# Kernel optimization log

Measured on AMD Instinct MI355X. Metric: run time of the kernel, lower is better.

## Reference

```python
import jax, jax.numpy as jnp
import numpy as np

EPS_COS = 1e-12
EPS_BN = 1e-5


def setup_inputs() -> dict:
    key = jax.random.key(0)
    k1, k2, k3 = jax.random.split(key, 3)
    B, C, H, W = 16384, 3, 32, 32
    K, NUM_CLASSES = 300, 10
    return {
        "x": jax.random.normal(k1, (B, C, H, W), dtype=jnp.float32),
        "w5": jax.random.normal(k2, (K, C, H, W), dtype=jnp.float32),
        "gamma": jnp.ones((K,), dtype=jnp.float32),
        "beta": jnp.zeros((K,), dtype=jnp.float32),
        "w6": jax.random.normal(k3, (NUM_CLASSES, K), dtype=jnp.float32),
    }


def _clp_cos_sim(x, w5):
    # kernel covers the full spatial extent -> one patch per sample.
    B = x.shape[0]
    K = w5.shape[0]
    xf = x.reshape(B, -1)                       # (B, C*H*W)
    wf = w5.reshape(K, -1)                      # (K, C*H*W)
    xn = xf / (jnp.linalg.norm(xf, axis=1, keepdims=True) + EPS_COS)
    wn = wf / (jnp.linalg.norm(wf, axis=1, keepdims=True) + EPS_COS)
    cos = jnp.einsum("bd,kd->bk", xn, wn)      # cosine similarity to each prototype
    return jax.nn.relu(cos)                     # clp: clamp negatives to 0


def reference(x, w5, gamma, beta, w6):
    # fc5: clamped cosine-similarity match against 300 prototypes -> (B, 300, 1, 1)
    fc5 = _clp_cos_sim(x, w5)[:, :, None, None]
    # bn5: BatchNorm2d(300), batch statistics (training-mode forward math)
    mean = jnp.mean(fc5, axis=(0, 2, 3), keepdims=True)
    var = jnp.var(fc5, axis=(0, 2, 3), keepdims=True)
    bn5 = gamma[None, :, None, None] * (fc5 - mean) / jnp.sqrt(var + EPS_BN) \
          + beta[None, :, None, None]
    # fc6: non-competitive 1x1 map 300 -> 10 (dot-product readout), flattened
    fc6 = jnp.einsum("bk,ok->bo", bn5[:, :, 0, 0], w6)   # (B, 10)
    return fc5, bn5, fc6
```

## Files before the change

### kernel.cpp

```cpp
#include <hip/hip_runtime.h>
#include <stdint.h>

#define BATCH 16384
#define DDIM  3072
#define NK    300
#define NKP   320
#define NCLS  10

#define BM 64
#define BN 320
#define BK 64
#define KT (DDIM / BK)

typedef __bf16 bf16x8 __attribute__((ext_vector_type(8)));
typedef float  f32x16 __attribute__((ext_vector_type(16)));

typedef __attribute__((address_space(1))) const void gvoid_as1;
typedef __attribute__((address_space(3))) void lvoid_as3;

__device__ __forceinline__ unsigned f2bf(float f) {
  unsigned u = __float_as_uint(f);
  u += 0x7FFFu + ((u >> 16) & 1u);
  return u >> 16;
}
__device__ __forceinline__ uint4 pack8bf(float4 a, float4 b) {
  uint4 p;
  p.x = f2bf(a.x) | (f2bf(a.y) << 16);
  p.y = f2bf(a.z) | (f2bf(a.w) << 16);
  p.z = f2bf(b.x) | (f2bf(b.y) << 16);
  p.w = f2bf(b.z) | (f2bf(b.w) << 16);
  return p;
}

__global__ __launch_bounds__(256) void prep_w_kernel(
    const float* __restrict__ w5, unsigned short* __restrict__ wn,
    float* __restrict__ rw, float* __restrict__ gsum, float* __restrict__ gsq) {
  const int r = blockIdx.x;
  const int t = threadIdx.x;
  if (r == 0) {
    for (int i = t; i < NKP; i += 256) { gsum[i] = 0.f; gsq[i] = 0.f; }
  }
  unsigned long long* dst = (unsigned long long*)(wn + (size_t)r * DDIM);
  if (r < NK) {
    const float4* src = (const float4*)(w5 + (size_t)r * DDIM);
    float ss = 0.f;
#pragma unroll
    for (int i = 0; i < 3; ++i) {
      float4 v = src[t + i * 256];
      ss += v.x * v.x + v.y * v.y + v.z * v.z + v.w * v.w;
      unsigned lo = f2bf(v.x) | (f2bf(v.y) << 16);
      unsigned hi = f2bf(v.z) | (f2bf(v.w) << 16);
      dst[t + i * 256] = (unsigned long long)lo | ((unsigned long long)hi << 32);
    }
#pragma unroll
    for (int m = 1; m <= 32; m <<= 1) ss += __shfl_xor(ss, m, 64);
    __shared__ float red[4];
    if ((t & 63) == 0) red[t >> 6] = ss;
    __syncthreads();
    if (t == 0) {
      float tot = red[0] + red[1] + red[2] + red[3];
      rw[r] = 1.f / (sqrtf(tot) + 1e-12f);
    }
  } else {
#pragma unroll
    for (int i = 0; i < 3; ++i) dst[t + i * 256] = 0ull;
    if (t == 0) rw[r] = 0.f;
  }
}

__global__ __launch_bounds__(320, 2) void gemm_kernel(
    const float* __restrict__ x, const unsigned short* __restrict__ wn,
    const float* __restrict__ rw, float* __restrict__ fc5,
    float* __restrict__ gsum, float* __restrict__ gsq) {
  __shared__ alignas(16) unsigned short xs[BM * BK];
  __shared__ alignas(16) unsigned short wt[BN * BK];
  __shared__ float rxs[BM];

  const int tid  = threadIdx.x;
  const int lane = tid & 63;
  const int w    = tid >> 6;
  const int m0   = (int)blockIdx.x * BM;

  const int srow = tid >> 2;
  const int sseg = tid & 3;
  const float* xsrc = x + (size_t)(m0 + srow) * DDIM + sseg * 16;
  const int wb0 = srow * 128 + ((((sseg << 1) | 0) ^ (srow & 7)) << 4);
  const int wb1 = srow * 128 + ((((sseg << 1) | 1) ^ (srow & 7)) << 4);

  const int wrow_l = lane >> 3;
  const int wchk_l = (lane & 7) ^ wrow_l;
  const unsigned short* wsrc_base = wn + (size_t)wrow_l * DDIM + wchk_l * 8;

  const int r31   = lane & 31;
  const int khalf = lane >> 5;
  const int rb0 = w * 64 + r31;
  const int rb1 = rb0 + 32;
  const char* aA0 = (const char*)xs + (size_t)r31 * 128;
  const char* aA1 = (const char*)xs + (size_t)(r31 + 32) * 128;
  const char* aB0 = (const char*)wt + (size_t)rb0 * 128;
  const char* aB1 = (const char*)wt + (size_t)rb1 * 128;
  const int swzA = r31 & 7;
  const int swzB0 = rb0 & 7, swzB1 = rb1 & 7;

  f32x16 acc00 = {}, acc01 = {}, acc10 = {}, acc11 = {};
  float ss = 0.f;

  float4 v0, v1, v2, v3;
  if (tid < 256) {
    const float4* p = (const float4*)xsrc;
    v0 = p[0]; v1 = p[1]; v2 = p[2]; v3 = p[3];
  }

  for (int kt = 0; kt < KT; ++kt) {
    if (tid < 256) {
      ss += v0.x*v0.x + v0.y*v0.y + v0.z*v0.z + v0.w*v0.w
          + v1.x*v1.x + v1.y*v1.y + v1.z*v1.z + v1.w*v1.w
          + v2.x*v2.x + v2.y*v2.y + v2.z*v2.z + v2.w*v2.w
          + v3.x*v3.x + v3.y*v3.y + v3.z*v3.z + v3.w*v3.w;
      *(uint4*)((char*)xs + wb0) = pack8bf(v0, v1);
      *(uint4*)((char*)xs + wb1) = pack8bf(v2, v3);
    }
#pragma unroll
    for (int j = 0; j < 8; ++j) {
      const int i = w * 8 + j;
      const unsigned short* src = wsrc_base + (size_t)(8 * i) * DDIM + kt * BK;
      __builtin_amdgcn_global_load_lds((gvoid_as1*)src,
                                       (lvoid_as3*)((char*)wt + i * 1024), 16, 0, 0);
    }
    __syncthreads();
    if (kt + 1 < KT && tid < 256) {
      const float4* p = (const float4*)(xsrc + (size_t)(kt + 1) * BK);
      v0 = p[0]; v1 = p[1]; v2 = p[2]; v3 = p[3];
    }
#pragma unroll
    for (int ks = 0; ks < 4; ++ks) {
      const int c16 = ks * 2 + khalf;
      bf16x8 a0 = *(const bf16x8*)(aA0 + ((c16 ^ swzA) << 4));
      bf16x8 a1 = *(const bf16x8*)(aA1 + ((c16 ^ swzA) << 4));
      bf16x8 b0 = *(const bf16x8*)(aB0 + ((c16 ^ swzB0) << 4));
      bf16x8 b1 = *(const bf16x8*)(aB1 + ((c16 ^ swzB1) << 4));
      acc00 = __builtin_amdgcn_mfma_f32_32x32x16_bf16(a0, b0, acc00, 0, 0, 0);
      acc01 = __builtin_amdgcn_mfma_f32_32x32x16_bf16(a0, b1, acc01, 0, 0, 0);
      acc10 = __builtin_amdgcn_mfma_f32_32x32x16_bf16(a1, b0, acc10, 0, 0, 0);
      acc11 = __builtin_amdgcn_mfma_f32_32x32x16_bf16(a1, b1, acc11, 0, 0, 0);
    }
    if (kt + 1 < KT) __syncthreads();
  }

  ss += __shfl_xor(ss, 1, 64);
  ss += __shfl_xor(ss, 2, 64);
  if (tid < 256 && sseg == 0) rxs[srow] = 1.f / (sqrtf(ss) + 1e-12f);
  __syncthreads();

  const int kh4 = khalf * 4;
  const int ng0 = w * 64 + r31;
  const int ng1 = ng0 + 32;
  const float rwv0 = rw[ng0];
  const float rwv1 = rw[ng1];
  float s0 = 0.f, q0 = 0.f, s1 = 0.f, q1 = 0.f;

#define EPI(ACC, MI, NG, RWV, SV, QV)                                         \
  _Pragma("unroll")                                                           \
  for (int r = 0; r < 16; ++r) {                                              \
    const int row = MI * 32 + (r & 3) + 8 * (r >> 2) + kh4;                   \
    float v = ACC[r] * rxs[row] * RWV;                                        \
    v = fmaxf(v, 0.f);                                                        \
    if (NG < NK) fc5[(size_t)(m0 + row) * NK + NG] = v;                       \
    SV += v; QV += v * v;                                                     \
  }
  EPI(acc00, 0, ng0, rwv0, s0, q0)
  EPI(acc01, 0, ng1, rwv1, s1, q1)
  EPI(acc10, 1, ng0, rwv0, s0, q0)
  EPI(acc11, 1, ng1, rwv1, s1, q1)
#undef EPI

  s0 += __shfl_xor(s0, 32, 64); q0 += __shfl_xor(q0, 32, 64);
  s1 += __shfl_xor(s1, 32, 64); q1 += __shfl_xor(q1, 32, 64);
  if (lane < 32) {
    atomicAdd(&gsum[ng0], s0); atomicAdd(&gsq[ng0], q0);
    if (ng1 < NK) { atomicAdd(&gsum[ng1], s1); atomicAdd(&gsq[ng1], q1); }
  }
}

__global__ __launch_bounds__(256) void bn_fc6_kernel(
    const float* __restrict__ fc5, const float* __restrict__ w6,
    const float* __restrict__ gamma, const float* __restrict__ beta,
    const float* __restrict__ gsum, const float* __restrict__ gsq,
    float* __restrict__ bn5, float* __restrict__ fc6) {
  __shared__ float w6s[NCLS * NK];
  __shared__ float scs[NK], shs[NK];
  const int t = threadIdx.x;
  for (int i = t; i < NCLS * NK; i += 256) w6s[i] = w6[i];
  for (int i = t; i < NK; i += 256) {
    const float invB = 1.f / (float)BATCH;
    float mean = gsum[i] * invB;
    float var  = gsq[i] * invB - mean * mean;
    var = fmaxf(var, 0.f);
    float sc = gamma[i] * rsqrtf(var + 1e-5f);
    scs[i] = sc;
    shs[i] = beta[i] - mean * sc;
  }
  __syncthreads();
  const int wv = t >> 6, l = t & 63;
  const int r = (int)blockIdx.x * 4 + wv;
  const float* frow = fc5 + (size_t)r * NK;
  float* brow = bn5 + (size_t)r * NK;
  float accv[NCLS];
#pragma unroll
  for (int o = 0; o < NCLS; ++o) accv[o] = 0.f;
#pragma unroll
  for (int i = 0; i < 5; ++i) {
    const int k = i * 64 + l;
    if (k < NK) {
      float b = frow[k] * scs[k] + shs[k];
      brow[k] = b;
#pragma unroll
      for (int o = 0; o < NCLS; ++o) accv[o] += b * w6s[o * NK + k];
    }
  }
#pragma unroll
  for (int o = 0; o < NCLS; ++o) {
    float v = accv[o];
#pragma unroll
    for (int m = 1; m <= 32; m <<= 1) v += __shfl_xor(v, m, 64);
    if (l == 0) fc6[(size_t)r * NCLS + o] = v;
  }
}

extern "C" void kernel_launch(void* const* d_in, const int* in_sizes, int n_in,
                              void* d_out, int out_size, void* d_ws, size_t ws_size,
                              hipStream_t stream) {
  const float* x     = (const float*)d_in[0];
  const float* w5    = (const float*)d_in[1];
  const float* gamma = (const float*)d_in[2];
  const float* beta  = (const float*)d_in[3];
  const float* w6    = (const float*)d_in[4];

  float* fc5 = (float*)d_out;
  float* bn5 = fc5 + (size_t)BATCH * NK;
  float* fc6 = bn5 + (size_t)BATCH * NK;

  char* ws = (char*)d_ws;
  unsigned short* wn = (unsigned short*)ws;
  float* rw   = (float*)(ws + (size_t)NKP * DDIM * 2);
  float* gsum = rw + NKP;
  float* gsq  = gsum + NKP;

  hipLaunchKernelGGL(prep_w_kernel, dim3(NKP), dim3(256), 0, stream,
                     w5, wn, rw, gsum, gsq);
  hipLaunchKernelGGL(gemm_kernel, dim3(BATCH / BM), dim3(320), 0, stream,
                     x, wn, rw, fc5, gsum, gsq);
  hipLaunchKernelGGL(bn_fc6_kernel, dim3(BATCH / 4), dim3(256), 0, stream,
                     fc5, w6, gamma, beta, gsum, gsq, bn5, fc6);
}
```

Measured before the change: 360.3 us.

## Halve GEMM row tile and load weight fragments directly from global memory

Shrinks the batch tile from 64 to 32 rows and uses 10 waves per block, each owning one 32-column MFMA tile. Weight fragments are read straight from global memory into registers instead of being staged in LDS via global_load_lds, which removes the weight LDS buffer. The aim is to raise occupancy and cut LDS traffic and pressure. The cost is double the total weight re-reads from L2, with no prefetch to hide that latency.

```diff
diff --git a/kernel.cpp b/kernel.cpp
--- a/kernel.cpp
+++ b/kernel.cpp
@@ -7,29 +7,17 @@
 #define NKP   320
 #define NCLS  10
 
-#define BM 64
-#define BN 320
+#define BM 32
 #define BK 64
 #define KT (DDIM / BK)
 
 typedef __bf16 bf16x8 __attribute__((ext_vector_type(8)));
 typedef float  f32x16 __attribute__((ext_vector_type(16)));
-
-typedef __attribute__((address_space(1))) const void gvoid_as1;
-typedef __attribute__((address_space(3))) void lvoid_as3;
 
 __device__ __forceinline__ unsigned f2bf(float f) {
   unsigned u = __float_as_uint(f);
   u += 0x7FFFu + ((u >> 16) & 1u);
   return u >> 16;
-}
-__device__ __forceinline__ uint4 pack8bf(float4 a, float4 b) {
-  uint4 p;
-  p.x = f2bf(a.x) | (f2bf(a.y) << 16);
-  p.y = f2bf(a.z) | (f2bf(a.w) << 16);
-  p.z = f2bf(b.x) | (f2bf(b.y) << 16);
-  p.w = f2bf(b.z) | (f2bf(b.w) << 16);
-  return p;
 }
 
 __global__ __launch_bounds__(256) void prep_w_kernel(
@@ -68,12 +56,11 @@
   }
 }
 
-__global__ __launch_bounds__(320, 2) void gemm_kernel(
+__global__ __launch_bounds__(640, 5) void gemm_kernel(
     const float* __restrict__ x, const unsigned short* __restrict__ wn,
     const float* __restrict__ rw, float* __restrict__ fc5,
     float* __restrict__ gsum, float* __restrict__ gsq) {
   __shared__ alignas(16) unsigned short xs[BM * BK];
-  __shared__ alignas(16) unsigned short wt[BN * BK];
   __shared__ float rxs[BM];
 
   const int tid  = threadIdx.x;
@@ -81,104 +68,76 @@
   const int w    = tid >> 6;
   const int m0   = (int)blockIdx.x * BM;
 
-  const int srow = tid >> 2;
-  const int sseg = tid & 3;
-  const float* xsrc = x + (size_t)(m0 + srow) * DDIM + sseg * 16;
-  const int wb0 = srow * 128 + ((((sseg << 1) | 0) ^ (srow & 7)) << 4);
-  const int wb1 = srow * 128 + ((((sseg << 1) | 1) ^ (srow & 7)) << 4);
-
-  const int wrow_l = lane >> 3;
-  const int wchk_l = (lane & 7) ^ wrow_l;
-  const unsigned short* wsrc_base = wn + (size_t)wrow_l * DDIM + wchk_l * 8;
+  const int srow = tid >> 4;
+  const int sseg = tid & 15;
+  const float* xsrc = x + (size_t)(m0 + srow) * DDIM + sseg * 4;
+  const int wbyte = srow * 128 + ((((sseg >> 1) ^ (srow & 7))) << 4) + ((sseg & 1) << 3);
 
   const int r31   = lane & 31;
   const int khalf = lane >> 5;
-  const int rb0 = w * 64 + r31;
-  const int rb1 = rb0 + 32;
-  const char* aA0 = (const char*)xs + (size_t)r31 * 128;
-  const char* aA1 = (const char*)xs + (size_t)(r31 + 32) * 128;
-  const char* aB0 = (const char*)wt + (size_t)rb0 * 128;
-  const char* aB1 = (const char*)wt + (size_t)rb1 * 128;
-  const int swzA = r31 & 7;
-  const int swzB0 = rb0 & 7, swzB1 = rb1 & 7;
-
-  f32x16 acc00 = {}, acc01 = {}, acc10 = {}, acc11 = {};
+  const int ng    = w * 32 + r31;
+  const unsigned short* bbase = wn + (size_t)ng * DDIM + khalf * 8;
+
+  const char* abase = (const char*)xs + (size_t)r31 * 128;
+  const int aswz = r31 & 7;
+
+  f32x16 acc = {};
   float ss = 0.f;
 
-  float4 v0, v1, v2, v3;
-  if (tid < 256) {
-    const float4* p = (const float4*)xsrc;
-    v0 = p[0]; v1 = p[1]; v2 = p[2]; v3 = p[3];
-  }
+  float4 v;
+  if (tid < 512) v = *(const float4*)xsrc;
 
   for (int kt = 0; kt < KT; ++kt) {
-    if (tid < 256) {
-      ss += v0.x*v0.x + v0.y*v0.y + v0.z*v0.z + v0.w*v0.w
-          + v1.x*v1.x + v1.y*v1.y + v1.z*v1.z + v1.w*v1.w
-          + v2.x*v2.x + v2.y*v2.y + v2.z*v2.z + v2.w*v2.w
-          + v3.x*v3.x + v3.y*v3.y + v3.z*v3.z + v3.w*v3.w;
-      *(uint4*)((char*)xs + wb0) = pack8bf(v0, v1);
-      *(uint4*)((char*)xs + wb1) = pack8bf(v2, v3);
-    }
-#pragma unroll
-    for (int j = 0; j < 8; ++j) {
-      const int i = w * 8 + j;
-      const unsigned short* src = wsrc_base + (size_t)(8 * i) * DDIM + kt * BK;
-      __builtin_amdgcn_global_load_lds((gvoid_as1*)src,
-                                       (lvoid_as3*)((char*)wt + i * 1024), 16, 0, 0);
+    if (tid < 512) {
+      ss += v.x * v.x + v.y * v.y + v.z * v.z + v.w * v.w;
+      unsigned lo = f2bf(v.x) | (f2bf(v.y) << 16);
+      unsigned hi = f2bf(v.z) | (f2bf(v.w) << 16);
+      *(unsigned long long*)((char*)xs + wbyte) =
+          (unsigned long long)lo | ((unsigned long long)hi << 32);
     }
     __syncthreads();
-    if (kt + 1 < KT && tid < 256) {
-      const float4* p = (const float4*)(xsrc + (size_t)(kt + 1) * BK);
-      v0 = p[0]; v1 = p[1]; v2 = p[2]; v3 = p[3];
-    }
-#pragma unroll
-    for (int ks = 0; ks < 4; ++ks) {
-      const int c16 = ks * 2 + khalf;
-      bf16x8 a0 = *(const bf16x8*)(aA0 + ((c16 ^ swzA) << 4));
-      bf16x8 a1 = *(const bf16x8*)(aA1 + ((c16 ^ swzA) << 4));
-      bf16x8 b0 = *(const bf16x8*)(aB0 + ((c16 ^ swzB0) << 4));
-      bf16x8 b1 = *(const bf16x8*)(aB1 + ((c16 ^ swzB1) << 4));
-      acc00 = __builtin_amdgcn_mfma_f32_32x32x16_bf16(a0, b0, acc00, 0, 0, 0);
-      acc01 = __builtin_amdgcn_mfma_f32_32x32x16_bf16(a0, b1, acc01, 0, 0, 0);
-      acc10 = __builtin_amdgcn_mfma_f32_32x32x16_bf16(a1, b0, acc10, 0, 0, 0);
-      acc11 = __builtin_amdgcn_mfma_f32_32x32x16_bf16(a1, b1, acc11, 0, 0, 0);
-    }
-    if (kt + 1 < KT) __syncthreads();
-  }
-
-  ss += __shfl_xor(ss, 1, 64);
-  ss += __shfl_xor(ss, 2, 64);
-  if (tid < 256 && sseg == 0) rxs[srow] = 1.f / (sqrtf(ss) + 1e-12f);
+    if (kt + 1 < KT && tid < 512) v = *(const float4*)(xsrc + (size_t)(kt + 1) * BK);
+    const unsigned short* bk = bbase + (size_t)kt * BK;
+    bf16x8 b0 = *(const bf16x8*)(bk + 0 * 16);
+    bf16x8 b1 = *(const bf16x8*)(bk + 1 * 16);
+    bf16x8 b2 = *(const bf16x8*)(bk + 2 * 16);
+    bf16x8 b3 = *(const bf16x8*)(bk + 3 * 16);
+    bf16x8 a0 = *(const bf16x8*)(abase + (((0 * 2 + khalf) ^ aswz) << 4));
+    bf16x8 a1 = *(const bf16x8*)(abase + (((1 * 2 + khalf) ^ aswz) << 4));
+    bf16x8 a2 = *(const bf16x8*)(abase + (((2 * 2 + khalf) ^ aswz) << 4));
+    bf16x8 a3 = *(const bf16x8*)(abase + (((3 * 2 + khalf) ^ aswz) << 4));
+    acc = __builtin_amdgcn_mfma_f32_32x32x16_bf16(a0, b0, acc, 0, 0, 0);
+    acc = __builtin_amdgcn_mfma_f32_32x32x16_bf16(a1, b1, acc, 0, 0, 0);
+    acc = __builtin_amdgcn_mfma_f32_32x32x16_bf16(a2, b2, acc, 0, 0, 0);
+    acc = __builtin_amdgcn_mfma_f32_32x32x16_bf16(a3, b3, acc, 0, 0, 0);
+    __syncthreads();
+  }
+
+  if (tid < 512) {
+    ss += __shfl_xor(ss, 1, 64);
+    ss += __shfl_xor(ss, 2, 64);
+    ss += __shfl_xor(ss, 4, 64);
+    ss += __shfl_xor(ss, 8, 64);
+    if ((tid & 15) == 0) rxs[srow] = 1.f / (sqrtf(ss) + 1e-12f);
+  }
   __syncthreads();
 
   const int kh4 = khalf * 4;
-  const int ng0 = w * 64 + r31;
-  const int ng1 = ng0 + 32;
-  const float rwv0 = rw[ng0];
-  const float rwv1 = rw[ng1];
-  float s0 = 0.f, q0 = 0.f, s1 = 0.f, q1 = 0.f;
-
-#define EPI(ACC, MI, NG, RWV, SV, QV)                                         \
-  _Pragma("unroll")                                                           \
-  for (int r = 0; r < 16; ++r) {                                              \
-    const int row = MI * 32 + (r & 3) + 8 * (r >> 2) + kh4;                   \
-    float v = ACC[r] * rxs[row] * RWV;                                        \
-    v = fmaxf(v, 0.f);                                                        \
-    if (NG < NK) fc5[(size_t)(m0 + row) * NK + NG] = v;                       \
-    SV += v; QV += v * v;                                                     \
-  }
-  EPI(acc00, 0, ng0, rwv0, s0, q0)
-  EPI(acc01, 0, ng1, rwv1, s1, q1)
-  EPI(acc10, 1, ng0, rwv0, s0, q0)
-  EPI(acc11, 1, ng1, rwv1, s1, q1)
-#undef EPI
-
-  s0 += __shfl_xor(s0, 32, 64); q0 += __shfl_xor(q0, 32, 64);
-  s1 += __shfl_xor(s1, 32, 64); q1 += __shfl_xor(q1, 32, 64);
-  if (lane < 32) {
-    atomicAdd(&gsum[ng0], s0); atomicAdd(&gsq[ng0], q0);
-    if (ng1 < NK) { atomicAdd(&gsum[ng1], s1); atomicAdd(&gsq[ng1], q1); }
+  const float rwv = (ng < NK) ? rw[ng] : 0.f;
+  float s = 0.f, q = 0.f;
+#pragma unroll
+  for (int r = 0; r < 16; ++r) {
+    const int row = (r & 3) + 8 * (r >> 2) + kh4;
+    float vv = acc[r] * rxs[row] * rwv;
+    vv = fmaxf(vv, 0.f);
+    if (ng < NK) fc5[(size_t)(m0 + row) * NK + ng] = vv;
+    s += vv; q += vv * vv;
+  }
+  s += __shfl_xor(s, 32, 64);
+  q += __shfl_xor(q, 32, 64);
+  if (lane < 32 && ng < NK) {
+    atomicAdd(&gsum[ng], s);
+    atomicAdd(&gsq[ng], q);
   }
 }
 
@@ -248,7 +207,7 @@
 
   hipLaunchKernelGGL(prep_w_kernel, dim3(NKP), dim3(256), 0, stream,
                      w5, wn, rw, gsum, gsq);
-  hipLaunchKernelGGL(gemm_kernel, dim3(BATCH / BM), dim3(320), 0, stream,
+  hipLaunchKernelGGL(gemm_kernel, dim3(BATCH / BM), dim3(640), 0, stream,
                      x, wn, rw, fc5, gsum, gsq);
   hipLaunchKernelGGL(bn_fc6_kernel, dim3(BATCH / 4), dim3(256), 0, stream,
                      fc5, w6, gamma, beta, gsum, gsq, bn5, fc6);
```

Result: slower. 423.4 us (+17.5%).
